# Kernel tuning notes

Measured on AMD Instinct MI355X. Metric: run time of the kernel, lower is better.

Reference implementation:

```python
import jax, jax.numpy as jnp
import numpy as np
import math

B, S, D, H = 4, 2048, 1024, 16
HD = D // H  # 64

def setup_inputs() -> dict:
    key = jax.random.key(0)
    ks = jax.random.split(key, 4)
    x = jax.random.normal(ks[0], (B, S, D), dtype=jnp.float32)
    # causal mask, True = attend (precomputed as in the original usage)
    mask = jnp.tril(jnp.ones((S, S), dtype=bool))[None, None, :, :]
    c_attn_w = jax.random.normal(ks[1], (D, 3 * D), dtype=jnp.float32) * 0.02
    c_attn_b = jnp.zeros((3 * D,), dtype=jnp.float32)
    c_proj_w = jax.random.normal(ks[2], (D, D), dtype=jnp.float32) * 0.02
    c_proj_b = jnp.zeros((D,), dtype=jnp.float32)
    return {"x": x, "mask": mask, "c_attn_w": c_attn_w, "c_attn_b": c_attn_b,
            "c_proj_w": c_proj_w, "c_proj_b": c_proj_b}

def reference(x, mask, c_attn_w, c_attn_b, c_proj_w, c_proj_b):
    b, s, d = x.shape
    # c_attn: Conv1D acts as Linear with transposed weight convention
    qkv = x @ c_attn_w + c_attn_b                      # [B,S,3D]
    q, k, v = jnp.split(qkv, 3, axis=-1)
    q = q.reshape(b, s, H, HD).transpose(0, 2, 1, 3)   # [B,H,S,hd]
    k = k.reshape(b, s, H, HD).transpose(0, 2, 1, 3)   # [B,H,S,hd]
    v = v.reshape(b, s, H, HD).transpose(0, 2, 1, 3)   # [B,H,S,hd]
    # scores, scale by sqrt(head_dim) (done unconditionally in _attn)
    w = jnp.einsum('bhqd,bhkd->bhqk', q, k) / math.sqrt(HD)
    # masked_fill_(1 - mask, -10000.0)
    w = jnp.where(mask, w, jnp.float32(-10000.0))
    w = jax.nn.softmax(w, axis=-1)                     # attn_dropout p=0
    a = jnp.einsum('bhqk,bhkd->bhqd', w, v)            # [B,H,S,hd]
    a = a.transpose(0, 2, 1, 3).reshape(b, s, d)       # merge heads
    out = a @ c_proj_w + c_proj_b                      # resid_dropout p=0
    return out
```

## Files before the change

### kernel.cpp

```cpp
#include <hip/hip_runtime.h>

#define SEQ  2048
#define DIM  1024
#define NH   16
#define HD   64
#define NB   4

typedef __bf16 bf16_t;
typedef bf16_t bf16x8 __attribute__((ext_vector_type(8)));
typedef bf16_t bf16x4 __attribute__((ext_vector_type(4)));
typedef float  floatx4 __attribute__((ext_vector_type(4)));

#define MFMA16(a, b, c) __builtin_amdgcn_mfma_f32_16x16x32_bf16((a), (b), (c), 0, 0, 0)

__device__ __forceinline__ void gl_lds16(const bf16_t* g, bf16_t* l) {
    __builtin_amdgcn_global_load_lds(
        (const __attribute__((address_space(1))) void*)g,
        (__attribute__((address_space(3))) void*)l,
        16, 0, 0);
}

__global__ __launch_bounds__(256) void prep(
    const float* __restrict__ x, bf16_t* __restrict__ xb,
    const float* __restrict__ wqkv, bf16_t* __restrict__ wqkvT,
    const float* __restrict__ wproj, bf16_t* __restrict__ wprojT) {
    const int bid = blockIdx.x, tid = threadIdx.x;
    if (bid < 8192) {
        const int i = (bid * 256 + tid) * 4;
        const float4 v = *(const float4*)(x + i);
        xb[i + 0] = (bf16_t)v.x;
        xb[i + 1] = (bf16_t)v.y;
        xb[i + 2] = (bf16_t)v.z;
        xb[i + 3] = (bf16_t)v.w;
        return;
    }
    __shared__ bf16_t t[32][33];
    const float* in;
    bf16_t* out;
    int R, C, bx, by;
    if (bid < 8192 + 3072) {
        const int idx = bid - 8192;
        in = wqkv; out = wqkvT; R = 1024; C = 3072;
        bx = idx % 96; by = idx / 96;
    } else {
        const int idx = bid - 11264;
        in = wproj; out = wprojT; R = 1024; C = 1024;
        bx = idx & 31; by = idx >> 5;
    }
    const int c0 = bx * 32, r0 = by * 32;
    const int tx = tid & 31, ty = tid >> 5;
#pragma unroll
    for (int i = 0; i < 32; i += 8)
        t[ty + i][tx] = (bf16_t)in[(r0 + ty + i) * C + c0 + tx];
    __syncthreads();
#pragma unroll
    for (int i = 0; i < 32; i += 8)
        out[(c0 + ty + i) * R + r0 + tx] = t[tx][ty + i];
}

template <int MODE>
__global__ __launch_bounds__(256, 2) void gemm128(
    const bf16_t* __restrict__ A, const bf16_t* __restrict__ Bt,
    const float* __restrict__ bias, int K,
    bf16_t* __restrict__ Qo, bf16_t* __restrict__ Ko, bf16_t* __restrict__ Vo,
    float* __restrict__ Co) {
    __shared__ __align__(16) bf16_t smem[MODE == 0 ? 128 * 136 : 128 * 64];
    bf16_t* Al = smem;
    bf16_t* Bl = smem + 128 * 32;

    const int tid = threadIdx.x;
    const int m0 = blockIdx.y * 128, n0 = blockIdx.x * 128;
    const int w = tid >> 6, lane = tid & 63;
    const int l15 = lane & 15, quad = lane >> 4;
    const int wm = (w & 1) * 64, wn = (w >> 1) * 64;

    floatx4 acc[4][4] = {};

    const bf16_t* aptr = A + (m0 + (tid >> 2)) * K + (tid & 3) * 8;
    const bf16_t* bptr = Bt + (n0 + (tid >> 2)) * K + (tid & 3) * 8;
    bf16_t* al = Al + tid * 8;
    bf16_t* bl = Bl + tid * 8;

    for (int k0 = 0; k0 < K; k0 += 32) {
        gl_lds16(aptr, al);
        gl_lds16(aptr + 64 * K, al + 2048);
        gl_lds16(bptr, bl);
        gl_lds16(bptr + 64 * K, bl + 2048);
        aptr += 32;
        bptr += 32;
        __syncthreads();

        bf16x8 af[4], bfr[4];
#pragma unroll
        for (int i = 0; i < 4; i++)
            af[i] = *(const bf16x8*)&Al[(wm + i * 16 + l15) * 32 + quad * 8];
#pragma unroll
        for (int j = 0; j < 4; j++)
            bfr[j] = *(const bf16x8*)&Bl[(wn + j * 16 + l15) * 32 + quad * 8];
#pragma unroll
        for (int i = 0; i < 4; i++)
#pragma unroll
            for (int j = 0; j < 4; j++)
                acc[i][j] = MFMA16(af[i], bfr[j], acc[i][j]);
        __syncthreads();
    }

    if (MODE == 0) {
        bf16_t* Cl = smem;
        const int which = n0 >> 10;
        const float qs = (which == 0) ? 0.125f : 1.0f;
#pragma unroll
        for (int j = 0; j < 4; j++) {
            const int ncol = wn + j * 16 + l15;
            const float bv = bias[n0 + ncol];
#pragma unroll
            for (int i = 0; i < 4; i++)
#pragma unroll
                for (int r = 0; r < 4; r++) {
                    const int mrow = wm + i * 16 + quad * 4 + r;
                    Cl[mrow * 136 + ncol] = (bf16_t)((acc[i][j][r] + bv) * qs);
                }
        }
        __syncthreads();

        if (which < 2) {
            const int row = tid >> 1, ch = (tid & 1) << 6;
            const int m = m0 + row, b = m >> 11, s = m & 2047;
            const int h = ((n0 & 1023) >> 6) + (ch >> 6);
            bf16_t* dst = (which == 0 ? Qo : Ko) + ((size_t)(b * NH + h) * SEQ + s) * HD;
            const bf16_t* src = Cl + row * 136 + ch;
#pragma unroll
            for (int g = 0; g < 8; g++)
                *(bf16x8*)(dst + g * 8) = *(const bf16x8*)(src + g * 8);
        } else {
            const int dl = tid & 127, sh = (tid >> 7) << 6;
            const int h = ((n0 & 1023) >> 6) + (dl >> 6), d = dl & 63;
            const int b = m0 >> 11, sbase = (m0 & 2047) + sh;
            bf16_t* dst = Vo + ((size_t)(b * NH + h) * HD + d) * SEQ + sbase;
#pragma unroll
            for (int g = 0; g < 8; g++) {
                bf16x8 tv;
#pragma unroll
                for (int e = 0; e < 8; e++)
                    tv[e] = Cl[(sh + g * 8 + e) * 136 + dl];
                *(bf16x8*)(dst + g * 8) = tv;
            }
        }
    } else {
#pragma unroll
        for (int j = 0; j < 4; j++) {
            const int n = n0 + wn + j * 16 + l15;
            const float bv = bias[n];
#pragma unroll
            for (int i = 0; i < 4; i++)
#pragma unroll
                for (int r = 0; r < 4; r++) {
                    const int m = m0 + wm + i * 16 + quad * 4 + r;
                    Co[m * 1024 + n] = acc[i][j][r] + bv;
                }
        }
    }
}

__global__ __launch_bounds__(256, 2) void attn2q(
    const bf16_t* __restrict__ Q, const bf16_t* __restrict__ Kg,
    const bf16_t* __restrict__ Vt, bf16_t* __restrict__ Aout) {
    __shared__ bf16_t Ks[2 * 64 * 64];
    __shared__ bf16_t Vs[2 * 64 * 64];
    __shared__ bf16_t Ps[128 * 64];

    const int bh = blockIdx.y;
    const int px = (blockIdx.x + (bh >> 3)) & 7;
    const int qtA = 15 - px, qtB = px;
    const int nkA = 2 * qtA + 2, nkB = 2 * qtB + 2;

    const int tid = threadIdx.x, w = tid >> 6, lane = tid & 63;
    const int l15 = lane & 15, quad = lane >> 4;
    const int b = bh >> 4, hd = bh & 15;
    const int xk = l15 & 7;

    bf16x8 aqA[2][2], aqB[2][2];
#pragma unroll
    for (int i = 0; i < 2; i++) {
        const bf16_t* qrA = Q + (size_t)(bh * SEQ + qtA * 128 + w * 32 + i * 16 + l15) * HD;
        const bf16_t* qrB = Q + (size_t)(bh * SEQ + qtB * 128 + w * 32 + i * 16 + l15) * HD;
#pragma unroll
        for (int h = 0; h < 2; h++) {
            aqA[i][h] = *(const bf16x8*)(qrA + h * 32 + quad * 8);
            aqB[i][h] = *(const bf16x8*)(qrB + h * 32 + quad * 8);
        }
    }

    floatx4 oA[2][4] = {}, oB[2][4] = {};
    float liA[2] = {}, liB[2] = {};

    const int r_st = tid >> 2, g0 = tid & 3;
    const bf16_t* kgl = Kg + (size_t)bh * SEQ * HD + (size_t)r_st * HD;
    const bf16_t* vgl = Vt + (size_t)bh * HD * SEQ + (size_t)r_st * SEQ;
    const int sw0 = ((g0 ^ (r_st & 7)) * 8);
    const int sw1 = (((g0 + 4) ^ (r_st & 7)) * 8);

    auto proc = [&](int qt, bf16x8 (&aq)[2][2], floatx4 (&o)[2][4],
                    float (&li)[2], int kt, int sub) {
        const bf16_t* Ksub = Ks + sub * 4096;
        const bf16_t* Vsub = Vs + sub * 4096;
        bf16x8 bk[4][2];
#pragma unroll
        for (int j = 0; j < 4; j++) {
            const int n = j * 16 + l15;
#pragma unroll
            for (int h = 0; h < 2; h++)
                bk[j][h] = *(const bf16x8*)&Ksub[n * 64 + (((h * 4 + quad) ^ xk) * 8)];
        }
        floatx4 z[2][4] = {};
#pragma unroll
        for (int i = 0; i < 2; i++)
#pragma unroll
            for (int j = 0; j < 4; j++) {
                z[i][j] = MFMA16(bk[j][0], aq[i][0], z[i][j]);
                z[i][j] = MFMA16(bk[j][1], aq[i][1], z[i][j]);
            }
#pragma unroll
        for (int i = 0; i < 2; i++) {
            const int qbase = qt * 128 + w * 32 + i * 16;
            const int qrow_l = qbase + l15;
            const bool full = (kt * 64 + 63) <= qbase;
            const int prow = w * 32 + i * 16 + l15;
            bf16_t* pbase = Ps + prow * 64;
            const int rx = prow & 7;
#pragma unroll
            for (int j = 0; j < 4; j++) {
                const int kg0 = kt * 64 + j * 16 + quad * 4;
                bf16x4 pk;
#pragma unroll
                for (int r = 0; r < 4; r++) {
                    float e = __expf(z[i][j][r]);
                    if (!full && kg0 + r > qrow_l) e = 0.f;
                    li[i] += e;
                    pk[r] = (bf16_t)e;
                }
                const int g = 2 * j + (quad >> 1);
                *(bf16x4*)(pbase + (((g ^ rx) << 3) | ((quad & 1) << 2))) = pk;
            }
        }
        __builtin_amdgcn_s_waitcnt(0xC07F);
        bf16x8 ap[2][2];
#pragma unroll
        for (int i = 0; i < 2; i++) {
            const int row = w * 32 + i * 16 + l15;
#pragma unroll
            for (int kk = 0; kk < 2; kk++)
                ap[i][kk] = *(const bf16x8*)&Ps[row * 64 +
                                               (((kk * 4 + quad) ^ (row & 7)) << 3)];
        }
        bf16x8 bv[4][2];
#pragma unroll
        for (int j = 0; j < 4; j++) {
            const int n = j * 16 + l15;
#pragma unroll
            for (int kk = 0; kk < 2; kk++)
                bv[j][kk] = *(const bf16x8*)&Vsub[n * 64 + (((kk * 4 + quad) ^ xk) * 8)];
        }
#pragma unroll
        for (int i = 0; i < 2; i++)
#pragma unroll
            for (int j = 0; j < 4; j++) {
                o[i][j] = MFMA16(ap[i][0], bv[j][0], o[i][j]);
                o[i][j] = MFMA16(ap[i][1], bv[j][1], o[i][j]);
            }
    };

    for (int ktp = 0; ktp < nkA; ktp += 2) {
#pragma unroll
        for (int sub = 0; sub < 2; ++sub) {
            const int kt = ktp + sub;
            const bf16x8 k0 = *(const bf16x8*)(kgl + kt * 64 * HD + g0 * 8);
            const bf16x8 k1 = *(const bf16x8*)(kgl + kt * 64 * HD + (g0 + 4) * 8);
            const bf16x8 v0 = *(const bf16x8*)(vgl + kt * 64 + g0 * 8);
            const bf16x8 v1 = *(const bf16x8*)(vgl + kt * 64 + (g0 + 4) * 8);
            bf16_t* ks = Ks + sub * 4096 + r_st * 64;
            bf16_t* vs = Vs + sub * 4096 + r_st * 64;
            *(bf16x8*)(ks + sw0) = k0;
            *(bf16x8*)(ks + sw1) = k1;
            *(bf16x8*)(vs + sw0) = v0;
            *(bf16x8*)(vs + sw1) = v1;
        }
        __syncthreads();
#pragma unroll
        for (int sub = 0; sub < 2; ++sub) {
            const int kt = ktp + sub;
            proc(qtA, aqA, oA, liA, kt, sub);
            if (kt < nkB) proc(qtB, aqB, oB, liB, kt, sub);
        }
        __syncthreads();
    }

#pragma unroll
    for (int t = 0; t < 2; t++) {
        const int qt = t == 0 ? qtA : qtB;
        floatx4(&o)[2][4] = t == 0 ? oA : oB;
        float(&li)[2] = t == 0 ? liA : liB;
#pragma unroll
        for (int i = 0; i < 2; i++) {
            float s = li[i];
            s += __shfl_xor(s, 16, 64);
            s += __shfl_xor(s, 32, 64);
#pragma unroll
            for (int r = 0; r < 4; r++) {
                const float sv = __shfl(s, quad * 4 + r, 64);
                const float inv = 1.0f / sv;
                const int srow = qt * 128 + w * 32 + i * 16 + quad * 4 + r;
                bf16_t* orow = Aout + (size_t)(b * SEQ + srow) * DIM + hd * HD;
#pragma unroll
                for (int j = 0; j < 4; j++)
                    orow[j * 16 + l15] = (bf16_t)(o[i][j][r] * inv);
            }
        }
    }
}

extern "C" void kernel_launch(void* const* d_in, const int* in_sizes, int n_in,
                              void* d_out, int out_size, void* d_ws, size_t ws_size,
                              hipStream_t stream) {
    const float* x        = (const float*)d_in[0];
    const float* c_attn_w = (const float*)d_in[2];
    const float* c_attn_b = (const float*)d_in[3];
    const float* c_proj_w = (const float*)d_in[4];
    const float* c_proj_b = (const float*)d_in[5];
    float* out = (float*)d_out;

    char* ws = (char*)d_ws;
    bf16_t* xb     = (bf16_t*)ws; ws += (size_t)NB * SEQ * DIM * 2;
    bf16_t* wqkvT  = (bf16_t*)ws; ws += (size_t)3072 * 1024 * 2;
    bf16_t* wprojT = (bf16_t*)ws; ws += (size_t)1024 * 1024 * 2;
    bf16_t* Qb  = (bf16_t*)ws; ws += (size_t)NB * NH * SEQ * HD * 2;
    bf16_t* Kb  = (bf16_t*)ws; ws += (size_t)NB * NH * SEQ * HD * 2;
    bf16_t* Vtb = (bf16_t*)ws; ws += (size_t)NB * NH * SEQ * HD * 2;
    bf16_t* Ab  = (bf16_t*)ws; ws += (size_t)NB * SEQ * DIM * 2;

    prep<<<12288, 256, 0, stream>>>(x, xb, c_attn_w, wqkvT, c_proj_w, wprojT);

    gemm128<0><<<dim3(24, 64), 256, 0, stream>>>(xb, wqkvT, c_attn_b, 1024,
                                                 Qb, Kb, Vtb, nullptr);

    attn2q<<<dim3(8, NB * NH), 256, 0, stream>>>(Qb, Kb, Vtb, Ab);

    gemm128<1><<<dim3(8, 64), 256, 0, stream>>>(Ab, wprojT, c_proj_b, 1024,
                                                nullptr, nullptr, nullptr, out);
}
```

Baseline: 278.7 us.

## Double GEMM K-step to 64 with swizzled LDS layout and packed epilogue stores

The GEMM main loop now loads a 64-wide K slice per iteration instead of 32, halving the number of barriers per K. The global-to-LDS load assignment is rotated per row so that fragment reads from the 64-element LDS rows are spread across banks. For the QKV mode, the MFMA operands are swapped so each lane holds four consecutive output columns, which lets the epilogue write packed bf16x4 values to LDS instead of scalars. LDS use per block grows, which may reduce occupancy for the output-projection mode.

```diff
diff --git a/kernel.cpp b/kernel.cpp
--- a/kernel.cpp
+++ b/kernel.cpp
@@ -64,9 +64,9 @@
     const float* __restrict__ bias, int K,
     bf16_t* __restrict__ Qo, bf16_t* __restrict__ Ko, bf16_t* __restrict__ Vo,
     float* __restrict__ Co) {
-    __shared__ __align__(16) bf16_t smem[MODE == 0 ? 128 * 136 : 128 * 64];
+    __shared__ __align__(16) bf16_t smem[MODE == 0 ? 128 * 136 : 128 * 128];
     bf16_t* Al = smem;
-    bf16_t* Bl = smem + 128 * 32;
+    bf16_t* Bl = smem + 128 * 64;
 
     const int tid = threadIdx.x;
     const int m0 = blockIdx.y * 128, n0 = blockIdx.x * 128;
@@ -76,32 +76,39 @@
 
     floatx4 acc[4][4] = {};
 
-    const bf16_t* aptr = A + (m0 + (tid >> 2)) * K + (tid & 3) * 8;
-    const bf16_t* bptr = Bt + (n0 + (tid >> 2)) * K + (tid & 3) * 8;
+    const int g_st = ((tid & 7) - (tid >> 3)) & 7;
+    const bf16_t* aptr = A + (m0 + (tid >> 3)) * K + g_st * 8;
+    const bf16_t* bptr = Bt + (n0 + (tid >> 3)) * K + g_st * 8;
     bf16_t* al = Al + tid * 8;
     bf16_t* bl = Bl + tid * 8;
 
-    for (int k0 = 0; k0 < K; k0 += 32) {
-        gl_lds16(aptr, al);
-        gl_lds16(aptr + 64 * K, al + 2048);
-        gl_lds16(bptr, bl);
-        gl_lds16(bptr + 64 * K, bl + 2048);
-        aptr += 32;
-        bptr += 32;
-        __syncthreads();
-
-        bf16x8 af[4], bfr[4];
-#pragma unroll
-        for (int i = 0; i < 4; i++)
-            af[i] = *(const bf16x8*)&Al[(wm + i * 16 + l15) * 32 + quad * 8];
-#pragma unroll
-        for (int j = 0; j < 4; j++)
-            bfr[j] = *(const bf16x8*)&Bl[(wn + j * 16 + l15) * 32 + quad * 8];
-#pragma unroll
-        for (int i = 0; i < 4; i++)
+    for (int k0 = 0; k0 < K; k0 += 64) {
+#pragma unroll
+        for (int c = 0; c < 4; c++) {
+            gl_lds16(aptr + (c * 32) * K, al + c * 2048);
+            gl_lds16(bptr + (c * 32) * K, bl + c * 2048);
+        }
+        aptr += 64;
+        bptr += 64;
+        __syncthreads();
+
+#pragma unroll
+        for (int h = 0; h < 2; h++) {
+            const int sAB = (((h << 2) + quad + (l15 & 7)) & 7) * 8;
+            bf16x8 af[4], bfr[4];
+#pragma unroll
+            for (int i = 0; i < 4; i++)
+                af[i] = *(const bf16x8*)&Al[(wm + i * 16 + l15) * 64 + sAB];
 #pragma unroll
             for (int j = 0; j < 4; j++)
-                acc[i][j] = MFMA16(af[i], bfr[j], acc[i][j]);
+                bfr[j] = *(const bf16x8*)&Bl[(wn + j * 16 + l15) * 64 + sAB];
+#pragma unroll
+            for (int i = 0; i < 4; i++)
+#pragma unroll
+                for (int j = 0; j < 4; j++)
+                    acc[i][j] = MODE == 0 ? MFMA16(bfr[j], af[i], acc[i][j])
+                                          : MFMA16(af[i], bfr[j], acc[i][j]);
+        }
         __syncthreads();
     }
 
@@ -111,15 +118,16 @@
         const float qs = (which == 0) ? 0.125f : 1.0f;
 #pragma unroll
         for (int j = 0; j < 4; j++) {
-            const int ncol = wn + j * 16 + l15;
-            const float bv = bias[n0 + ncol];
-#pragma unroll
-            for (int i = 0; i < 4; i++)
-#pragma unroll
-                for (int r = 0; r < 4; r++) {
-                    const int mrow = wm + i * 16 + quad * 4 + r;
-                    Cl[mrow * 136 + ncol] = (bf16_t)((acc[i][j][r] + bv) * qs);
-                }
+            const int nc = wn + j * 16 + quad * 4;
+#pragma unroll
+            for (int i = 0; i < 4; i++) {
+                const int mrow = wm + i * 16 + l15;
+                bf16x4 pk;
+#pragma unroll
+                for (int r = 0; r < 4; r++)
+                    pk[r] = (bf16_t)((acc[i][j][r] + bias[n0 + nc + r]) * qs);
+                *(bf16x4*)&Cl[mrow * 136 + nc] = pk;
+            }
         }
         __syncthreads();
 
```

Result: faster. 256.0 us (-8.1%).
